# Optimization experiments

Hardware: AMD Instinct MI355X
Metric: run time of the kernel (lower is better)

## Reference

```python
import jax, jax.numpy as jnp
import numpy as np

N = 50_000      # node_num
E = 1_600_000   # n_edges (avg degree 32)
D = 256         # input feature dim
H = 128         # GCN / hidden units
FC = 1024       # fc0 units
C = 16          # num_classes


def _tn(key, shape, std=0.1):
    # truncated normal in [-2, 2] std, matching tf.random.truncated_normal(stddev=0.1)
    return jax.random.truncated_normal(key, -2.0, 2.0, shape, jnp.float32) * std


def setup_inputs() -> dict:
    key = jax.random.key(0)
    ks = jax.random.split(key, 16)
    return {
        "x": jax.random.normal(ks[0], (N, D), jnp.float32),
        "edge_index": jax.random.randint(ks[1], (2, E), 0, N, jnp.int32),
        # GCN layer params (tfg GCN: kernel + bias)
        "gcn0_W": _tn(ks[2], (D, H)), "gcn0_b": jnp.zeros((H,), jnp.float32),
        "gcn1_W": _tn(ks[3], (H, H)), "gcn1_b": jnp.zeros((H,), jnp.float32),
        "gcn2_W": _tn(ks[4], (H, H)), "gcn2_b": jnp.zeros((H,), jnp.float32),
        # extra dense block between gcn10 and gcn11
        "w1": _tn(ks[5], (H, H)), "b1": _tn(ks[6], (N, H)),
        # fc head
        "fc0_W": _tn(ks[7], (H, FC)), "fc0_b": jnp.zeros((FC,), jnp.float32),
        "fc1_W": _tn(ks[8], (FC, C)), "fc1_b": jnp.zeros((C,), jnp.float32),
    }


def reference(x, edge_index, gcn0_W, gcn0_b, gcn1_W, gcn1_b, gcn2_W, gcn2_b,
              w1, b1, fc0_W, fc0_b, fc1_W, fc1_b):
    n = x.shape[0]
    src, dst = edge_index[0], edge_index[1]
    loops = jnp.arange(n, dtype=src.dtype)
    # GCN renormalization trick: A_hat = A + I, w_ij = deg_i^-1/2 * deg_j^-1/2
    src_f = jnp.concatenate([src, loops])   # [E+N]
    dst_f = jnp.concatenate([dst, loops])
    deg = jax.ops.segment_sum(jnp.ones(src_f.shape[0], jnp.float32), src_f, num_segments=n)
    norm = jnp.where(deg > 0, deg, 1.0) ** -0.5
    ew = norm[src_f] * norm[dst_f]          # [E+N]

    def gcn(h, W, b):
        h = h @ W                                                      # [N,H]
        agg = jax.ops.segment_sum(h[src_f] * ew[:, None], dst_f, num_segments=n)
        return agg + b

    h1 = jax.nn.relu(gcn(x, gcn0_W, gcn0_b))       # gcn10, relu
    h11 = jax.nn.relu(h1 @ w1 + b1)                # dense with per-node bias
    h2 = gcn(h11, gcn1_W, gcn1_b)                  # gcn11, no activation
    h2 = jax.nn.relu(gcn(h2, gcn2_W, gcn2_b))      # gcn12, relu
    h = h1 + h2
    h = jax.nn.relu(h @ fc0_W + fc0_b)             # fc0
    return h @ fc1_W + fc1_b                       # fc1 logits [N,C]
```

## Files before the change

kernel.cpp:

```cpp
#include <hip/hip_runtime.h>
#include <hip/hip_bf16.h>
#include <hip/hip_fp16.h>
#include <cstddef>
#include <cstdint>

#define NNODES 50000
#define NEDGES 1600000
#define DIM 256
#define HID 128
#define FCU 1024
#define NCLS 16

#define NBKT 256
#define BW 196
#define NBLK_A 64
#define EPB (NEDGES / NBLK_A)
#define CAPB 8192

#define DCHUNK 12800
#define DSLICE 64
#define DEPB (NEDGES / DSLICE)

typedef short s16x8 __attribute__((ext_vector_type(8)));
typedef _Float16 f16x8 __attribute__((ext_vector_type(8)));
typedef float f32x4 __attribute__((ext_vector_type(4)));
#define MFMA16 __builtin_amdgcn_mfma_f32_16x16x32_bf16
#define MFMAH  __builtin_amdgcn_mfma_f32_16x16x32_f16

typedef unsigned short u16;
typedef unsigned int u32;

__device__ inline u16 f2bf(float f) {
    u32 u = __float_as_uint(f);
    return (u16)((u + 0x7FFF + ((u >> 16) & 1)) >> 16);
}
__device__ inline float bf2f(u16 h) { return __uint_as_float(((u32)h) << 16); }
__device__ inline void split2(float v, u16& h, u16& l) {
    h = f2bf(v);
    l = f2bf(v - bf2f(h));
}


__global__ __launch_bounds__(256) void histDeg(const int* __restrict__ ei, int* __restrict__ degS) {
    __shared__ int h[DCHUNK];
    int chunk = blockIdx.x >> 6;
    int slice = blockIdx.x & (DSLICE - 1);
    int t = threadIdx.x;
    int base0 = chunk * DCHUNK;
    for (int i = t; i < DCHUNK; i += 256) h[i] = 0;
    __syncthreads();
    int base = slice * DEPB;
    for (int e = base + t; e < base + DEPB; e += 256) {
        int s = ei[e] - base0;
        if ((unsigned)s < (unsigned)DCHUNK) atomicAdd(&h[s], 1);
    }
    __syncthreads();
    int lim = NNODES - base0; if (lim > DCHUNK) lim = DCHUNK;
    for (int i = t; i < lim; i += 256) {
        int v = h[i];
        if (v) atomicAdd(&degS[base0 + i], v);
    }
}

__global__ void norm_kernel(const int* __restrict__ degS, float* __restrict__ nrm) {
    int i = blockIdx.x * blockDim.x + threadIdx.x;
    if (i < NNODES) nrm[i] = rsqrtf((float)(degS[i] + 1));
}

__global__ __launch_bounds__(1024) void histA(const int* __restrict__ ei, int* __restrict__ hist) {
    __shared__ int h[NBKT];
    int blk = blockIdx.x, t = threadIdx.x;
    if (t < NBKT) h[t] = 0;
    __syncthreads();
    int base = blk * EPB;
    for (int e = base + t; e < base + EPB; e += 1024) {
        int dst = ei[NEDGES + e];
        atomicAdd(&h[dst / BW], 1);
    }
    __syncthreads();
    if (t < NBKT) hist[t * NBLK_A + blk] = h[t];
}

__global__ __launch_bounds__(1024) void scanh_a(int* __restrict__ hist, int* __restrict__ bsum) {
    __shared__ int s[1024];
    int b = blockIdx.x, t = threadIdx.x, i = b * 1024 + t;
    int v = hist[i];
    s[t] = v;
    __syncthreads();
    for (int off = 1; off < 1024; off <<= 1) {
        int x = (t >= off) ? s[t - off] : 0;
        __syncthreads();
        s[t] += x;
        __syncthreads();
    }
    hist[i] = s[t] - v;
    if (t == 1023) bsum[b] = s[1023];
}
__global__ void scanh_b(int* __restrict__ bsum) {
    if (threadIdx.x == 0 && blockIdx.x == 0) {
        int a = 0;
        for (int j = 0; j < 16; ++j) { int t = bsum[j]; bsum[j] = a; a += t; }
    }
}
__global__ __launch_bounds__(1024) void scanh_c(int* __restrict__ hist, const int* __restrict__ bsum) {
    int i = blockIdx.x * 1024 + threadIdx.x;
    hist[i] += bsum[blockIdx.x];
}

__global__ __launch_bounds__(1024) void bucket_fill(const int* __restrict__ ei,
                                                    const int* __restrict__ hist,
                                                    u32* __restrict__ packed) {
    __shared__ int cur[NBKT];
    int blk = blockIdx.x, t = threadIdx.x;
    if (t < NBKT) cur[t] = hist[t * NBLK_A + blk];
    __syncthreads();
    int base = blk * EPB;
    for (int e = base + t; e < base + EPB; e += 1024) {
        int src = ei[e], dst = ei[NEDGES + e];
        int p = atomicAdd(&cur[dst / BW], 1);
        packed[p] = ((u32)dst << 16) | (u32)src;
    }
}

__global__ __launch_bounds__(256) void bucket_csr(const u32* __restrict__ packed,
                                                  const int* __restrict__ hist,
                                                  int* __restrict__ rowptr, u16* __restrict__ csr) {
    __shared__ u32 st[CAPB];
    __shared__ u16 so[CAPB];
    __shared__ int cnt[256], excl[256];
    int b = blockIdx.x, t = threadIdx.x;
    int ebase = hist[b * NBLK_A];
    int eend  = (b < NBKT - 1) ? hist[(b + 1) * NBLK_A] : NEDGES;
    int nE = eend - ebase;
    if (nE > CAPB) nE = CAPB;
    cnt[t] = 0;
    __syncthreads();
    for (int i = t; i < nE; i += 256) {
        u32 p = packed[ebase + i];
        st[i] = p;
        atomicAdd(&cnt[(int)(p >> 16) - b * BW], 1);
    }
    __syncthreads();
    int v = cnt[t];
    excl[t] = v;
    __syncthreads();
    for (int off = 1; off < 256; off <<= 1) {
        int x = (t >= off) ? excl[t - off] : 0;
        __syncthreads();
        excl[t] += x;
        __syncthreads();
    }
    int ex = excl[t] - v;
    int node = b * BW + t;
    if (t < BW && node < NNODES) rowptr[node] = ebase + ex;
    if (b == NBKT - 1 && t == 0) rowptr[NNODES] = NEDGES;
    cnt[t] = ex;
    __syncthreads();
    for (int i = t; i < nE; i += 256) {
        u32 p = st[i];
        int pos = atomicAdd(&cnt[(int)(p >> 16) - b * BW], 1);
        so[pos] = (u16)(p & 0xFFFF);
    }
    __syncthreads();
    for (int i = t; i < nE; i += 256) csr[ebase + i] = so[i];
}


__global__ __launch_bounds__(256) void conv_x(const float* __restrict__ x,
                                              u16* __restrict__ xh, u16* __restrict__ xl) {
    int i = blockIdx.x * blockDim.x + threadIdx.x;
    const float4 v = *reinterpret_cast<const float4*>(x + (size_t)i * 4);
    u16 h0, l0, h1, l1, h2, l2, h3, l3;
    split2(v.x, h0, l0); split2(v.y, h1, l1); split2(v.z, h2, l2); split2(v.w, h3, l3);
    ushort4 hv = make_ushort4(h0, h1, h2, h3), lv = make_ushort4(l0, l1, l2, l3);
    *reinterpret_cast<ushort4*>(xh + (size_t)i * 4) = hv;
    *reinterpret_cast<ushort4*>(xl + (size_t)i * 4) = lv;
}

__global__ __launch_bounds__(256) void conv_wT(const float* __restrict__ W, int K, int N,
                                               u16* __restrict__ outH, u16* __restrict__ outL) {
    int o = blockIdx.x * blockDim.x + threadIdx.x;
    if (o < K * N) {
        int n = o / K, k = o - n * K;
        u16 h, l;
        split2(W[(size_t)k * N + n], h, l);
        outH[o] = h; outL[o] = l;
    }
}

__global__ __launch_bounds__(256) void conv_w1h(const float* __restrict__ W, __half* __restrict__ outT) {
    int o = blockIdx.x * blockDim.x + threadIdx.x;
    if (o < FCU * NCLS) {
        int n = o / FCU, k = o - n * FCU;
        outT[o] = __float2half(W[(size_t)k * NCLS + n]);
    }
}


template<int VAR>
__global__ __launch_bounds__(256) void agg_fast(
    const __half* __restrict__ g, const float* __restrict__ nrm,
    const int* __restrict__ rowptr, const u16* __restrict__ csr,
    const float* __restrict__ bias,
    const u16* __restrict__ h1H, const u16* __restrict__ h1L,
    u16* __restrict__ outH, u16* __restrict__ outL)
{
    int w = threadIdx.x >> 6, lane = threadIdx.x & 63;
    int i = blockIdx.x * 4 + w;
    if (i >= NNODES) return;
    const __half2* gp = reinterpret_cast<const __half2*>(g);
    size_t lrow = (size_t)i * 64 + lane;
    float2 acc = __half22float2(gp[lrow]);
    int e0 = rowptr[i], e1 = rowptr[i + 1];
    int e = e0;
    for (; e + 8 <= e1; e += 8) {
        int s[8];
#pragma unroll
        for (int q = 0; q < 8; ++q) s[q] = csr[e + q];
        __half2 v[8];
#pragma unroll
        for (int q = 0; q < 8; ++q) v[q] = gp[(size_t)s[q] * 64 + lane];
#pragma unroll
        for (int q = 0; q < 8; ++q) {
            float2 f = __half22float2(v[q]);
            acc.x += f.x; acc.y += f.y;
        }
    }
    for (; e < e1; ++e) {
        int s = csr[e];
        float2 f = __half22float2(gp[(size_t)s * 64 + lane]);
        acc.x += f.x; acc.y += f.y;
    }
    float ni = nrm[i];
    const float2 b = *reinterpret_cast<const float2*>(bias + lane * 2);
    float v0 = fmaf(ni, acc.x, b.x);
    float v1 = fmaf(ni, acc.y, b.y);
    if (VAR != 1) { v0 = fmaxf(v0, 0.f); v1 = fmaxf(v1, 0.f); }
    if (VAR == 2) {
        ushort2 rh = *reinterpret_cast<const ushort2*>(h1H + (size_t)i * HID + lane * 2);
        ushort2 rl = *reinterpret_cast<const ushort2*>(h1L + (size_t)i * HID + lane * 2);
        v0 += bf2f(rh.x) + bf2f(rl.x);
        v1 += bf2f(rh.y) + bf2f(rl.y);
    }
    u16 h0, l0, h1v, l1v;
    split2(v0, h0, l0);
    split2(v1, h1v, l1v);
    *reinterpret_cast<ushort2*>(outH + (size_t)i * HID + lane * 2) = make_ushort2(h0, h1v);
    *reinterpret_cast<ushort2*>(outL + (size_t)i * HID + lane * 2) = make_ushort2(l0, l1v);
}


template<int K, int MODE>
__global__ __launch_bounds__(256) void gemm_split(
    const u16* __restrict__ Ah, const u16* __restrict__ Al,
    const u16* __restrict__ BTh, const u16* __restrict__ BTl,
    const float* __restrict__ pnb, const float* __restrict__ nrmv,
    __half* __restrict__ outG, u16* __restrict__ outH, u16* __restrict__ outL, int M)
{
    const int PK = 40;
    __shared__ __align__(16) u16 AsH[64 * PK], AsL[64 * PK];
    __shared__ __align__(16) u16 BsH[128 * PK], BsL[128 * PK];
    int tid = threadIdx.x, lane = tid & 63, w = tid >> 6;
    int wr = w >> 1, wc = w & 1;
    int l15 = lane & 15, l4 = lane >> 4;
    int blockRow = blockIdx.x * 64;
    f32x4 acc[2][4] = {};

    for (int kk = 0; kk < K; kk += 32) {
        {
            int row = tid >> 2, kc = (tid & 3) * 8;
            int gr = blockRow + row; if (gr >= M) gr = M - 1;
            *(s16x8*)&AsH[row * PK + kc] = *(const s16x8*)&Ah[(size_t)gr * K + kk + kc];
            *(s16x8*)&AsL[row * PK + kc] = *(const s16x8*)&Al[(size_t)gr * K + kk + kc];
        }
#pragma unroll
        for (int i2 = 0; i2 < 2; ++i2) {
            int idx = tid + i2 * 256;
            int n = idx >> 2, kc = (idx & 3) * 8;
            *(s16x8*)&BsH[n * PK + kc] = *(const s16x8*)&BTh[(size_t)n * K + kk + kc];
            *(s16x8*)&BsL[n * PK + kc] = *(const s16x8*)&BTl[(size_t)n * K + kk + kc];
        }
        __syncthreads();
        s16x8 ah[2], al[2], bh[4], bl[4];
#pragma unroll
        for (int mi = 0; mi < 2; ++mi) {
            ah[mi] = *(const s16x8*)&AsH[(wr * 32 + mi * 16 + l15) * PK + 8 * l4];
            al[mi] = *(const s16x8*)&AsL[(wr * 32 + mi * 16 + l15) * PK + 8 * l4];
        }
#pragma unroll
        for (int ni = 0; ni < 4; ++ni) {
            bh[ni] = *(const s16x8*)&BsH[(wc * 64 + ni * 16 + l15) * PK + 8 * l4];
            bl[ni] = *(const s16x8*)&BsL[(wc * 64 + ni * 16 + l15) * PK + 8 * l4];
        }
#pragma unroll
        for (int mi = 0; mi < 2; ++mi)
#pragma unroll
            for (int ni = 0; ni < 4; ++ni) {
                acc[mi][ni] = MFMA16(ah[mi], bh[ni], acc[mi][ni], 0, 0, 0);
                acc[mi][ni] = MFMA16(ah[mi], bl[ni], acc[mi][ni], 0, 0, 0);
                acc[mi][ni] = MFMA16(al[mi], bh[ni], acc[mi][ni], 0, 0, 0);
            }
        __syncthreads();
    }
#pragma unroll
    for (int mi = 0; mi < 2; ++mi)
#pragma unroll
        for (int ni = 0; ni < 4; ++ni) {
            int c = wc * 64 + ni * 16 + l15;
#pragma unroll
            for (int j = 0; j < 4; ++j) {
                int r = blockRow + wr * 32 + mi * 16 + l4 * 4 + j;
                if (r < M) {
                    if (MODE == 0) {
                        outG[(size_t)r * 128 + c] = __float2half(nrmv[r] * acc[mi][ni][j]);
                    } else {
                        float v = fmaxf(acc[mi][ni][j] + pnb[(size_t)r * 128 + c], 0.f);
                        u16 h, l;
                        split2(v, h, l);
                        outH[(size_t)r * 128 + c] = h;
                        outL[(size_t)r * 128 + c] = l;
                    }
                }
            }
        }
}


__global__ __launch_bounds__(256) void fc_kernel(
    const u16* __restrict__ Ahi,
    const u16* __restrict__ BTh,
    const float* __restrict__ fc0b,
    const __half* __restrict__ W1f,
    const float* __restrict__ fc1b,
    float* __restrict__ out, int M)
{
    __shared__ __align__(16) u16 vs[32 * 128];
    __shared__ __align__(16) u16 W1s[16 * 128];
    int tid = threadIdx.x, lane = tid & 63, w = tid >> 6;
    int l15 = lane & 15, l4 = lane >> 4;
    int blockRow = blockIdx.x * 32;

    s16x8 ahr[2][4];
#pragma unroll
    for (int mi = 0; mi < 2; ++mi) {
        int r = blockRow + mi * 16 + l15; if (r >= M) r = M - 1;
#pragma unroll
        for (int ks = 0; ks < 4; ++ks)
            ahr[mi][ks] = *(const s16x8*)&Ahi[(size_t)r * HID + ks * 32 + 8 * l4];
    }

    f32x4 acc2 = {0.f, 0.f, 0.f, 0.f};
    s16x8 bcur[2][4];
#pragma unroll
    for (int ni = 0; ni < 2; ++ni)
#pragma unroll
        for (int ks = 0; ks < 4; ++ks)
            bcur[ni][ks] = *(const s16x8*)&BTh[(size_t)(w * 32 + ni * 16 + l15) * HID + ks * 32 + 8 * l4];

#pragma unroll
    for (int cc = 0; cc < FCU / 128; ++cc) {
        int co = cc * 128;
        s16x8 bnxt[2][4];
        if (cc + 1 < FCU / 128) {
#pragma unroll
            for (int ni = 0; ni < 2; ++ni)
#pragma unroll
                for (int ks = 0; ks < 4; ++ks)
                    bnxt[ni][ks] = *(const s16x8*)&BTh[(size_t)(co + 128 + w * 32 + ni * 16 + l15) * HID + ks * 32 + 8 * l4];
        }

        f32x4 acc[2][2] = {};
#pragma unroll
        for (int ks = 0; ks < 4; ++ks)
#pragma unroll
            for (int mi = 0; mi < 2; ++mi)
#pragma unroll
                for (int ni = 0; ni < 2; ++ni)
                    acc[mi][ni] = MFMA16(ahr[mi][ks], bcur[ni][ks], acc[mi][ni], 0, 0, 0);

        {
            int cls = tid >> 4, kc = (tid & 15) * 8;
            s16x8 t = *(const s16x8*)&W1f[(size_t)cls * FCU + co + kc];
            *(s16x8*)&W1s[cls * 128 + (kc ^ ((cls & 7) << 3))] = t;
        }
#pragma unroll
        for (int mi = 0; mi < 2; ++mi)
#pragma unroll
            for (int ni = 0; ni < 2; ++ni) {
                int unit = w * 32 + ni * 16 + l15;
                float b0v = fc0b[co + unit];
#pragma unroll
                for (int j = 0; j < 4; ++j) {
                    int rl = mi * 16 + l4 * 4 + j;
                    float v = fmaxf(acc[mi][ni][j] + b0v, 0.f);
                    vs[rl * 128 + (unit ^ ((rl & 7) << 3))] = __half_as_ushort(__float2half(v));
                }
            }
        __syncthreads();

        if (w < 2) {
#pragma unroll
            for (int ks = 0; ks < 4; ++ks) {
                int row = w * 16 + l15;
                int colk = ks * 32 + 8 * l4;
                f16x8 a2 = *(const f16x8*)&vs[row * 128 + (colk ^ ((row & 7) << 3))];
                f16x8 b2 = *(const f16x8*)&W1s[l15 * 128 + (colk ^ ((l15 & 7) << 3))];
                acc2 = MFMAH(a2, b2, acc2, 0, 0, 0);
            }
        }
        __syncthreads();

        if (cc + 1 < FCU / 128) {
#pragma unroll
            for (int ni = 0; ni < 2; ++ni)
#pragma unroll
                for (int ks = 0; ks < 4; ++ks)
                    bcur[ni][ks] = bnxt[ni][ks];
        }
    }

    if (w < 2) {
#pragma unroll
        for (int j = 0; j < 4; ++j) {
            int gr = blockRow + w * 16 + l4 * 4 + j;
            if (gr < M) out[(size_t)gr * NCLS + l15] = acc2[j] + fc1b[l15];
        }
    }
}


extern "C" void kernel_launch(void* const* d_in, const int* in_sizes, int n_in,
                              void* d_out, int out_size, void* d_ws, size_t ws_size,
                              hipStream_t stream)
{
    const float* x     = (const float*)d_in[0];
    const int*   ei    = (const int*)d_in[1];
    const float* gcn0W = (const float*)d_in[2];
    const float* gcn0b = (const float*)d_in[3];
    const float* gcn1W = (const float*)d_in[4];
    const float* gcn1b = (const float*)d_in[5];
    const float* gcn2W = (const float*)d_in[6];
    const float* gcn2b = (const float*)d_in[7];
    const float* w1    = (const float*)d_in[8];
    const float* b1    = (const float*)d_in[9];
    const float* fc0W  = (const float*)d_in[10];
    const float* fc0b  = (const float*)d_in[11];
    const float* fc1W  = (const float*)d_in[12];
    const float* fc1b  = (const float*)d_in[13];
    float* out = (float*)d_out;

    char* ws = (char*)d_ws;
    size_t off = 0;
    auto alloc = [&](size_t bytes) -> void* {
        void* p = ws + off;
        off = (off + bytes + 255) & ~(size_t)255;
        return p;
    };
    int* degS   = (int*)alloc((size_t)NNODES * 4);
    int* rowptr = (int*)alloc((size_t)(NNODES + 1) * 4);
    int* hist   = (int*)alloc((size_t)NBKT * NBLK_A * 4);
    int* bsum   = (int*)alloc(64 * 4);
    u32* packed = (u32*)alloc((size_t)NEDGES * 4);
    u16* csr    = (u16*)alloc((size_t)NEDGES * 2);
    float* nrm  = (float*)alloc((size_t)NNODES * 4);
    u16* W0Th = (u16*)alloc((size_t)DIM * HID * 2);  u16* W0Tl = (u16*)alloc((size_t)DIM * HID * 2);
    u16* w1Th = (u16*)alloc((size_t)HID * HID * 2);  u16* w1Tl = (u16*)alloc((size_t)HID * HID * 2);
    u16* W1Th = (u16*)alloc((size_t)HID * HID * 2);  u16* W1Tl = (u16*)alloc((size_t)HID * HID * 2);
    u16* W2Th = (u16*)alloc((size_t)HID * HID * 2);  u16* W2Tl = (u16*)alloc((size_t)HID * HID * 2);
    u16* F0Th = (u16*)alloc((size_t)HID * FCU * 2);  u16* F0Tl = (u16*)alloc((size_t)HID * FCU * 2);
    __half* W1f = (__half*)alloc((size_t)FCU * NCLS * 2);
    __half* bufG = (__half*)alloc((size_t)NNODES * HID * 2);
    u16* R1 = (u16*)alloc((size_t)2 * NNODES * DIM * 2);
    u16* xh = R1, *xl = R1 + (size_t)NNODES * DIM;
    u16* h1H = R1,                            *h1L = R1 + (size_t)NNODES * HID;
    u16* B3H = R1 + (size_t)2 * NNODES * HID, *B3L = R1 + (size_t)3 * NNODES * HID;

    const int M = NNODES;
    hipMemsetAsync(degS, 0, (size_t)NNODES * 4, stream);

    histDeg<<<4 * DSLICE, 256, 0, stream>>>(ei, degS);
    norm_kernel<<<(NNODES + 255) / 256, 256, 0, stream>>>(degS, nrm);
    histA<<<NBLK_A, 1024, 0, stream>>>(ei, hist);
    scanh_a<<<16, 1024, 0, stream>>>(hist, bsum);
    scanh_b<<<1, 64, 0, stream>>>(bsum);
    scanh_c<<<16, 1024, 0, stream>>>(hist, bsum);
    bucket_fill<<<NBLK_A, 1024, 0, stream>>>(ei, hist, packed);
    bucket_csr<<<NBKT, 256, 0, stream>>>(packed, hist, rowptr, csr);

    conv_x<<<(NNODES * DIM / 4 + 255) / 256, 256, 0, stream>>>(x, xh, xl);
    conv_wT<<<(DIM * HID + 255) / 256, 256, 0, stream>>>(gcn0W, DIM, HID, W0Th, W0Tl);
    conv_wT<<<(HID * HID + 255) / 256, 256, 0, stream>>>(w1,    HID, HID, w1Th, w1Tl);
    conv_wT<<<(HID * HID + 255) / 256, 256, 0, stream>>>(gcn1W, HID, HID, W1Th, W1Tl);
    conv_wT<<<(HID * HID + 255) / 256, 256, 0, stream>>>(gcn2W, HID, HID, W2Th, W2Tl);
    conv_wT<<<(HID * FCU + 255) / 256, 256, 0, stream>>>(fc0W,  HID, FCU, F0Th, F0Tl);
    conv_w1h<<<(FCU * NCLS + 255) / 256, 256, 0, stream>>>(fc1W, W1f);

    const int GB = (M + 63) / 64;
    const int GB32 = (M + 31) / 32;
    const int AB = (NNODES + 3) / 4;
    gemm_split<DIM, 0><<<GB, 256, 0, stream>>>(xh, xl, W0Th, W0Tl, nullptr, nrm, bufG, nullptr, nullptr, M);
    agg_fast<0><<<AB, 256, 0, stream>>>(bufG, nrm, rowptr, csr, gcn0b, nullptr, nullptr, h1H, h1L);
    gemm_split<HID, 1><<<GB, 256, 0, stream>>>(h1H, h1L, w1Th, w1Tl, b1, nullptr, nullptr, B3H, B3L, M);
    gemm_split<HID, 0><<<GB, 256, 0, stream>>>(B3H, B3L, W1Th, W1Tl, nullptr, nrm, bufG, nullptr, nullptr, M);
    agg_fast<1><<<AB, 256, 0, stream>>>(bufG, nrm, rowptr, csr, gcn1b, nullptr, nullptr, B3H, B3L);
    gemm_split<HID, 0><<<GB, 256, 0, stream>>>(B3H, B3L, W2Th, W2Tl, nullptr, nrm, bufG, nullptr, nullptr, M);
    agg_fast<2><<<AB, 256, 0, stream>>>(bufG, nrm, rowptr, csr, gcn2b, h1H, h1L, B3H, B3L);
    fc_kernel<<<GB32, 256, 0, stream>>>(B3H, F0Th, fc0b, W1f, fc1b, out, M);
}
```

Measured before the change: 432.6 us.

## Partition CSR by source-chunk windows and aggregate 8 nodes per wave by window

The CSR build now sorts each destination's edges into four source-range chunks of 12800 nodes and records four row pointers per node. The aggregation kernel processes 8 destination nodes per wave and iterates over the source windows in the outer loop. This aims to keep gathered feature rows within a smaller working set so they hit L2/MALL more often. In exchange each wave does more serial work, the gather unroll drops to 4, there are fewer waves overall, and the row-pointer array is four times larger.

```diff
diff --git a/kernel.cpp b/kernel.cpp
--- a/kernel.cpp
+++ b/kernel.cpp
@@ -13,6 +13,7 @@
 
 #define NBKT 256
 #define BW 196
+#define BW4 (BW * 4)
 #define NBLK_A 64
 #define EPB (NEDGES / NBLK_A)
 #define CAPB 8192
@@ -124,42 +125,57 @@
 
 __global__ __launch_bounds__(256) void bucket_csr(const u32* __restrict__ packed,
                                                   const int* __restrict__ hist,
-                                                  int* __restrict__ rowptr, u16* __restrict__ csr) {
+                                                  int* __restrict__ rowptr4, u16* __restrict__ csr) {
     __shared__ u32 st[CAPB];
     __shared__ u16 so[CAPB];
-    __shared__ int cnt[256], excl[256];
+    __shared__ int cnt2[BW4];
+    __shared__ int tsum[256];
     int b = blockIdx.x, t = threadIdx.x;
     int ebase = hist[b * NBLK_A];
     int eend  = (b < NBKT - 1) ? hist[(b + 1) * NBLK_A] : NEDGES;
     int nE = eend - ebase;
     if (nE > CAPB) nE = CAPB;
-    cnt[t] = 0;
+    for (int i = t; i < BW4; i += 256) cnt2[i] = 0;
     __syncthreads();
     for (int i = t; i < nE; i += 256) {
         u32 p = packed[ebase + i];
         st[i] = p;
-        atomicAdd(&cnt[(int)(p >> 16) - b * BW], 1);
-    }
-    __syncthreads();
-    int v = cnt[t];
-    excl[t] = v;
+        int dst = (int)(p >> 16), src = (int)(p & 0xFFFF);
+        atomicAdd(&cnt2[(dst - b * BW) * 4 + src / DCHUNK], 1);
+    }
+    __syncthreads();
+    int c0 = 0, c1 = 0, c2 = 0, c3 = 0, s0 = 0;
+    if (t < BW) {
+        c0 = cnt2[t * 4]; c1 = cnt2[t * 4 + 1]; c2 = cnt2[t * 4 + 2]; c3 = cnt2[t * 4 + 3];
+        s0 = c0 + c1 + c2 + c3;
+    }
+    tsum[t] = s0;
     __syncthreads();
     for (int off = 1; off < 256; off <<= 1) {
-        int x = (t >= off) ? excl[t - off] : 0;
-        __syncthreads();
-        excl[t] += x;
-        __syncthreads();
-    }
-    int ex = excl[t] - v;
-    int node = b * BW + t;
-    if (t < BW && node < NNODES) rowptr[node] = ebase + ex;
-    if (b == NBKT - 1 && t == 0) rowptr[NNODES] = NEDGES;
-    cnt[t] = ex;
+        int x = (t >= off) ? tsum[t - off] : 0;
+        __syncthreads();
+        tsum[t] += x;
+        __syncthreads();
+    }
+    int texcl = tsum[t] - s0;
+    if (t < BW) {
+        int o0 = texcl, o1 = texcl + c0, o2 = texcl + c0 + c1, o3 = texcl + c0 + c1 + c2;
+        cnt2[t * 4] = o0; cnt2[t * 4 + 1] = o1; cnt2[t * 4 + 2] = o2; cnt2[t * 4 + 3] = o3;
+        int node = b * BW + t;
+        if (node < NNODES) {
+            rowptr4[node * 4]     = ebase + o0;
+            rowptr4[node * 4 + 1] = ebase + o1;
+            rowptr4[node * 4 + 2] = ebase + o2;
+            rowptr4[node * 4 + 3] = ebase + o3;
+        }
+    }
+    if (b == NBKT - 1 && t == 0) rowptr4[4 * NNODES] = NEDGES;
     __syncthreads();
     for (int i = t; i < nE; i += 256) {
         u32 p = st[i];
-        int pos = atomicAdd(&cnt[(int)(p >> 16) - b * BW], 1);
-        so[pos] = (u16)(p & 0xFFFF);
+        int dst = (int)(p >> 16), src = (int)(p & 0xFFFF);
+        int pos = atomicAdd(&cnt2[(dst - b * BW) * 4 + src / DCHUNK], 1);
+        so[pos] = (u16)src;
     }
     __syncthreads();
     for (int i = t; i < nE; i += 256) csr[ebase + i] = so[i];
@@ -198,55 +214,67 @@
 
 
 template<int VAR>
-__global__ __launch_bounds__(256) void agg_fast(
+__global__ __launch_bounds__(256) void agg_win(
     const __half* __restrict__ g, const float* __restrict__ nrm,
-    const int* __restrict__ rowptr, const u16* __restrict__ csr,
+    const int* __restrict__ rowptr4, const u16* __restrict__ csr,
     const float* __restrict__ bias,
     const u16* __restrict__ h1H, const u16* __restrict__ h1L,
     u16* __restrict__ outH, u16* __restrict__ outL)
 {
-    int w = threadIdx.x >> 6, lane = threadIdx.x & 63;
-    int i = blockIdx.x * 4 + w;
-    if (i >= NNODES) return;
+    int wv = threadIdx.x >> 6, lane = threadIdx.x & 63;
+    int wid = blockIdx.x * 4 + wv;
+    if (wid >= NNODES / 8) return;
+    int base = wid * 8;
     const __half2* gp = reinterpret_cast<const __half2*>(g);
-    size_t lrow = (size_t)i * 64 + lane;
-    float2 acc = __half22float2(gp[lrow]);
-    int e0 = rowptr[i], e1 = rowptr[i + 1];
-    int e = e0;
-    for (; e + 8 <= e1; e += 8) {
-        int s[8];
-#pragma unroll
-        for (int q = 0; q < 8; ++q) s[q] = csr[e + q];
-        __half2 v[8];
-#pragma unroll
-        for (int q = 0; q < 8; ++q) v[q] = gp[(size_t)s[q] * 64 + lane];
-#pragma unroll
-        for (int q = 0; q < 8; ++q) {
-            float2 f = __half22float2(v[q]);
-            acc.x += f.x; acc.y += f.y;
-        }
-    }
-    for (; e < e1; ++e) {
-        int s = csr[e];
-        float2 f = __half22float2(gp[(size_t)s * 64 + lane]);
-        acc.x += f.x; acc.y += f.y;
-    }
-    float ni = nrm[i];
-    const float2 b = *reinterpret_cast<const float2*>(bias + lane * 2);
-    float v0 = fmaf(ni, acc.x, b.x);
-    float v1 = fmaf(ni, acc.y, b.y);
-    if (VAR != 1) { v0 = fmaxf(v0, 0.f); v1 = fmaxf(v1, 0.f); }
-    if (VAR == 2) {
-        ushort2 rh = *reinterpret_cast<const ushort2*>(h1H + (size_t)i * HID + lane * 2);
-        ushort2 rl = *reinterpret_cast<const ushort2*>(h1L + (size_t)i * HID + lane * 2);
-        v0 += bf2f(rh.x) + bf2f(rl.x);
-        v1 += bf2f(rh.y) + bf2f(rl.y);
-    }
-    u16 h0, l0, h1v, l1v;
-    split2(v0, h0, l0);
-    split2(v1, h1v, l1v);
-    *reinterpret_cast<ushort2*>(outH + (size_t)i * HID + lane * 2) = make_ushort2(h0, h1v);
-    *reinterpret_cast<ushort2*>(outL + (size_t)i * HID + lane * 2) = make_ushort2(l0, l1v);
+    float2 acc[8];
+#pragma unroll
+    for (int k = 0; k < 8; ++k) acc[k] = __half22float2(gp[(size_t)(base + k) * 64 + lane]);
+
+#pragma unroll 1
+    for (int w = 0; w < 4; ++w) {
+#pragma unroll
+        for (int k = 0; k < 8; ++k) {
+            int n4 = (base + k) * 4 + w;
+            int e0 = rowptr4[n4], e1 = rowptr4[n4 + 1];
+            int e = e0;
+            for (; e + 4 <= e1; e += 4) {
+                int s0c = csr[e], s1c = csr[e + 1], s2c = csr[e + 2], s3c = csr[e + 3];
+                __half2 v0 = gp[(size_t)s0c * 64 + lane];
+                __half2 v1 = gp[(size_t)s1c * 64 + lane];
+                __half2 v2 = gp[(size_t)s2c * 64 + lane];
+                __half2 v3 = gp[(size_t)s3c * 64 + lane];
+                float2 a0 = __half22float2(v0), a1 = __half22float2(v1);
+                float2 a2 = __half22float2(v2), a3 = __half22float2(v3);
+                acc[k].x += (a0.x + a1.x) + (a2.x + a3.x);
+                acc[k].y += (a0.y + a1.y) + (a2.y + a3.y);
+            }
+            for (; e < e1; ++e) {
+                float2 f = __half22float2(gp[(size_t)csr[e] * 64 + lane]);
+                acc[k].x += f.x; acc[k].y += f.y;
+            }
+        }
+    }
+
+    const float2 bb = *reinterpret_cast<const float2*>(bias + lane * 2);
+#pragma unroll
+    for (int k = 0; k < 8; ++k) {
+        int i = base + k;
+        float ni = nrm[i];
+        float v0 = fmaf(ni, acc[k].x, bb.x);
+        float v1 = fmaf(ni, acc[k].y, bb.y);
+        if (VAR != 1) { v0 = fmaxf(v0, 0.f); v1 = fmaxf(v1, 0.f); }
+        if (VAR == 2) {
+            ushort2 rh = *reinterpret_cast<const ushort2*>(h1H + (size_t)i * HID + lane * 2);
+            ushort2 rl = *reinterpret_cast<const ushort2*>(h1L + (size_t)i * HID + lane * 2);
+            v0 += bf2f(rh.x) + bf2f(rl.x);
+            v1 += bf2f(rh.y) + bf2f(rl.y);
+        }
+        u16 h0, l0, h1v, l1v;
+        split2(v0, h0, l0);
+        split2(v1, h1v, l1v);
+        *reinterpret_cast<ushort2*>(outH + (size_t)i * HID + lane * 2) = make_ushort2(h0, h1v);
+        *reinterpret_cast<ushort2*>(outL + (size_t)i * HID + lane * 2) = make_ushort2(l0, l1v);
+    }
 }
 
 
@@ -456,13 +484,13 @@
         off = (off + bytes + 255) & ~(size_t)255;
         return p;
     };
-    int* degS   = (int*)alloc((size_t)NNODES * 4);
-    int* rowptr = (int*)alloc((size_t)(NNODES + 1) * 4);
-    int* hist   = (int*)alloc((size_t)NBKT * NBLK_A * 4);
-    int* bsum   = (int*)alloc(64 * 4);
-    u32* packed = (u32*)alloc((size_t)NEDGES * 4);
-    u16* csr    = (u16*)alloc((size_t)NEDGES * 2);
-    float* nrm  = (float*)alloc((size_t)NNODES * 4);
+    int* degS    = (int*)alloc((size_t)NNODES * 4);
+    int* rowptr4 = (int*)alloc((size_t)(4 * NNODES + 4) * 4);
+    int* hist    = (int*)alloc((size_t)NBKT * NBLK_A * 4);
+    int* bsum    = (int*)alloc(64 * 4);
+    u32* packed  = (u32*)alloc((size_t)NEDGES * 4);
+    u16* csr     = (u16*)alloc((size_t)NEDGES * 2);
+    float* nrm   = (float*)alloc((size_t)NNODES * 4);
     u16* W0Th = (u16*)alloc((size_t)DIM * HID * 2);  u16* W0Tl = (u16*)alloc((size_t)DIM * HID * 2);
     u16* w1Th = (u16*)alloc((size_t)HID * HID * 2);  u16* w1Tl = (u16*)alloc((size_t)HID * HID * 2);
     u16* W1Th = (u16*)alloc((size_t)HID * HID * 2);  u16* W1Tl = (u16*)alloc((size_t)HID * HID * 2);
@@ -485,7 +513,7 @@
     scanh_b<<<1, 64, 0, stream>>>(bsum);
     scanh_c<<<16, 1024, 0, stream>>>(hist, bsum);
     bucket_fill<<<NBLK_A, 1024, 0, stream>>>(ei, hist, packed);
-    bucket_csr<<<NBKT, 256, 0, stream>>>(packed, hist, rowptr, csr);
+    bucket_csr<<<NBKT, 256, 0, stream>>>(packed, hist, rowptr4, csr);
 
     conv_x<<<(NNODES * DIM / 4 + 255) / 256, 256, 0, stream>>>(x, xh, xl);
     conv_wT<<<(DIM * HID + 255) / 256, 256, 0, stream>>>(gcn0W, DIM, HID, W0Th, W0Tl);
@@ -497,13 +525,13 @@
 
     const int GB = (M + 63) / 64;
     const int GB32 = (M + 31) / 32;
-    const int AB = (NNODES + 3) / 4;
+    const int AW = (NNODES / 8 + 3) / 4;
     gemm_split<DIM, 0><<<GB, 256, 0, stream>>>(xh, xl, W0Th, W0Tl, nullptr, nrm, bufG, nullptr, nullptr, M);
-    agg_fast<0><<<AB, 256, 0, stream>>>(bufG, nrm, rowptr, csr, gcn0b, nullptr, nullptr, h1H, h1L);
+    agg_win<0><<<AW, 256, 0, stream>>>(bufG, nrm, rowptr4, csr, gcn0b, nullptr, nullptr, h1H, h1L);
     gemm_split<HID, 1><<<GB, 256, 0, stream>>>(h1H, h1L, w1Th, w1Tl, b1, nullptr, nullptr, B3H, B3L, M);
     gemm_split<HID, 0><<<GB, 256, 0, stream>>>(B3H, B3L, W1Th, W1Tl, nullptr, nrm, bufG, nullptr, nullptr, M);
-    agg_fast<1><<<AB, 256, 0, stream>>>(bufG, nrm, rowptr, csr, gcn1b, nullptr, nullptr, B3H, B3L);
+    agg_win<1><<<AW, 256, 0, stream>>>(bufG, nrm, rowptr4, csr, gcn1b, nullptr, nullptr, B3H, B3L);
     gemm_split<HID, 0><<<GB, 256, 0, stream>>>(B3H, B3L, W2Th, W2Tl, nullptr, nrm, bufG, nullptr, nullptr, M);
-    agg_fast<2><<<AB, 256, 0, stream>>>(bufG, nrm, rowptr, csr, gcn2b, h1H, h1L, B3H, B3L);
+    agg_win<2><<<AW, 256, 0, stream>>>(bufG, nrm, rowptr4, csr, gcn2b, h1H, h1L, B3H, B3L);
     fc_kernel<<<GB32, 256, 0, stream>>>(B3H, F0Th, fc0b, W1f, fc1b, out, M);
 }
```

Result: slower. 512.1 us (+18.4%).
